# Optimization experiments

Hardware: AMD Instinct MI355X
Metric: run time of the kernel (lower is better)

The kernel has to match this reference:

```python
import jax, jax.numpy as jnp
import numpy as np

B, L, D = 1, 2048, 4096
H, KV, HD = 32, 8, 128
ROT = 64  # head_dim * partial_rotary_factor
SCALE = HD ** -0.5
NEG = -1e9


def _apply_rope(x, cos, sin):
    # x: [B, h, L, HD]; rotate only the first ROT dims (partial rotary, rotate-half convention)
    xr, xp = x[..., :ROT], x[..., ROT:]
    x1, x2 = jnp.split(xr, 2, axis=-1)
    rotated = jnp.concatenate([-x2, x1], axis=-1)
    xr = xr * cos[None, None] + rotated * sin[None, None]
    return jnp.concatenate([xr, xp], axis=-1)


def setup_inputs() -> dict:
    key = jax.random.key(0)
    k1, k2, k3 = jax.random.split(key, 3)
    x = jax.random.normal(k1, (B, L, D), jnp.float32)
    w_qkv = jax.random.normal(k2, (D, H * HD + 2 * KV * HD), jnp.float32) * 0.02
    w_o = jax.random.normal(k3, (H * HD, D), jnp.float32) * 0.02
    # causal additive mask, broadcast over batch and heads
    causal = jnp.tril(jnp.ones((L, L), dtype=bool))
    attention_mask = jnp.where(causal, 0.0, NEG).astype(jnp.float32)[None, None]
    # rotary tables over the ROT rotary dims
    inv_freq = 1.0 / (10000.0 ** (jnp.arange(0, ROT, 2, dtype=jnp.float32) / ROT))
    t = jnp.arange(L, dtype=jnp.float32)
    freqs = jnp.outer(t, inv_freq)            # [L, ROT/2]
    emb = jnp.concatenate([freqs, freqs], -1)  # [L, ROT]
    cos, sin = jnp.cos(emb), jnp.sin(emb)
    return {"x": x, "attention_mask": attention_mask, "cos": cos, "sin": sin,
            "w_qkv": w_qkv, "w_o": w_o}


def reference(x, attention_mask, cos, sin, w_qkv, w_o):
    Bx, Lx, _ = x.shape
    qkv = x @ w_qkv                                   # [B, L, H*HD + 2*KV*HD]
    q_pos = H * HD
    kv_pos = q_pos + KV * HD
    q = qkv[:, :, :q_pos].reshape(Bx, Lx, H, HD).transpose(0, 2, 1, 3)
    k = qkv[:, :, q_pos:kv_pos].reshape(Bx, Lx, KV, HD).transpose(0, 2, 1, 3)
    v = qkv[:, :, kv_pos:].reshape(Bx, Lx, KV, HD).transpose(0, 2, 1, 3)
    q = _apply_rope(q, cos, sin)
    k = _apply_rope(k, cos, sin)
    # GQA: duplicate KV heads (as in the original module)
    n_rep = H // KV
    k = jnp.repeat(k, n_rep, axis=1)
    v = jnp.repeat(v, n_rep, axis=1)
    w = jnp.einsum("bhqd,bhkd->bhqk", q, k) * SCALE   # [B, H, L, L]
    w = jax.nn.softmax(w + attention_mask, axis=-1)
    o = jnp.einsum("bhqk,bhkd->bhqd", w, v)           # [B, H, L, HD]
    o = o.transpose(0, 2, 1, 3).reshape(Bx, Lx, H * HD)
    return o @ w_o
```

## Files before the change

kernel.cpp:

```cpp
#include <hip/hip_runtime.h>
#include <stdint.h>

typedef float f32x4 __attribute__((ext_vector_type(4)));
typedef short s16x8 __attribute__((ext_vector_type(8)));
typedef unsigned short u16x4 __attribute__((ext_vector_type(4)));

#define SCALE_F 0.08838834764831845f

__device__ __forceinline__ unsigned short f32_to_bf16(float f) {
    union { float f; unsigned int u; } v; v.f = f;
    return (unsigned short)((v.u + 0x7FFFu + ((v.u >> 16) & 1u)) >> 16);
}

__device__ __forceinline__ void gload16(const void* g, void* l) {
    __builtin_amdgcn_global_load_lds((const __attribute__((address_space(1))) unsigned int*)g,
                                     (__attribute__((address_space(3))) unsigned int*)l,
                                     16, 0, 0);
}

__global__ void k_conv_bf16(const float* __restrict__ in, unsigned short* __restrict__ out, int n4) {
    int i = blockIdx.x * 256 + threadIdx.x;
    if (i >= n4) return;
    f32x4 v = ((const f32x4*)in)[i];
    u16x4 o;
    o[0] = f32_to_bf16(v[0]); o[1] = f32_to_bf16(v[1]);
    o[2] = f32_to_bf16(v[2]); o[3] = f32_to_bf16(v[3]);
    ((u16x4*)out)[i] = o;
}

__global__ void k_transpose_bf16(const float* __restrict__ in, unsigned short* __restrict__ out,
                                 int R, int in_ld, int in_off) {
    __shared__ float tile[64][65];
    const int rb = blockIdx.y * 64, cb = blockIdx.x * 64;
    const int t = threadIdx.x;
    const int lr = t >> 4, lc4 = (t & 15) * 4;
#pragma unroll
    for (int i = 0; i < 4; ++i) {
        int r = i * 16 + lr;
        f32x4 v = *(const f32x4*)(in + (size_t)(rb + r) * in_ld + in_off + cb + lc4);
        tile[r][lc4 + 0] = v[0]; tile[r][lc4 + 1] = v[1];
        tile[r][lc4 + 2] = v[2]; tile[r][lc4 + 3] = v[3];
    }
    __syncthreads();
#pragma unroll
    for (int i = 0; i < 4; ++i) {
        int oc = cb + i * 16 + lr;
        u16x4 o;
#pragma unroll
        for (int j = 0; j < 4; ++j)
            o[j] = f32_to_bf16(tile[lc4 + j][i * 16 + lr]);
        *(u16x4*)(out + (size_t)oc * R + rb + lc4) = o;
    }
}

template<int BN>
__global__ __launch_bounds__(512, 1)
void k_gemm8p(const unsigned short* __restrict__ A, const unsigned short* __restrict__ Bt,
              float* __restrict__ C, int N, int K) {
    constexpr int BH = BN * 32;
    constexpr int NF = BN / 64;
    __shared__ __align__(16) unsigned short As[2][2][8192];
    __shared__ __align__(16) unsigned short Bs[2][2][BH];
    const int tid = threadIdx.x;
    const int lane = tid & 63, wid = tid >> 6;
    const int g = lane >> 4, l15 = lane & 15;
    const int wm = wid >> 2, wn = wid & 3;
    const int nwg = gridDim.x, bid = blockIdx.x;
    const int swz = (bid & 7) * (nwg >> 3) + (bid >> 3);
    const int ntn = N / BN;
    const int bm = swz / ntn, bn = swz - bm * ntn;
    const int brow = bm << 8, bcol = bn * BN;

    const int rowS = ((tid >> 6) << 4) | (tid & 15);
    const int kcS = (tid >> 4) & 3;
    const unsigned short* sA = A + (size_t)(brow + rowS) * K + kcS * 8;
    const unsigned short* sB = Bt + (size_t)(bcol + rowS) * K + kcS * 8;

    f32x4 acc[8][NF] = {};
    const int nt = K >> 6;

    auto stA = [&](int t, int kh) {
        unsigned short* d = &As[t & 1][kh][tid * 8];
        const unsigned short* s = sA + (size_t)t * 64 + kh * 32;
        gload16(s, d);
        gload16(s + (size_t)128 * K, d + 4096);
    };
    auto stB = [&](int t, int kh) {
        unsigned short* d = &Bs[t & 1][kh][tid * 8];
        const unsigned short* s = sB + (size_t)t * 64 + kh * 32;
        gload16(s, d);
        if constexpr (BN == 256) gload16(s + (size_t)128 * K, d + 4096);
    };

    stA(0, 0); stB(0, 0); stA(0, 1); stB(0, 1);

    for (int t = 0; t < nt; ++t) {
        const int c = t & 1;
        if constexpr (BN == 256) {
            s16x8 af[4], bf[4];
            if (t + 1 < nt) { stA(t + 1, 0); asm volatile("s_waitcnt vmcnt(6)" ::: "memory"); }
            else            { asm volatile("s_waitcnt vmcnt(4)" ::: "memory"); }
            __builtin_amdgcn_s_barrier();
#pragma unroll
            for (int f = 0; f < 4; ++f)
                af[f] = *(const s16x8*)(&As[c][0][((wm * 8 + f) * 64 + g * 16 + l15) * 8]);
#pragma unroll
            for (int j = 0; j < 4; ++j)
                bf[j] = *(const s16x8*)(&Bs[c][0][((wn * 4 + j) * 64 + g * 16 + l15) * 8]);
            __builtin_amdgcn_s_setprio(1);
#pragma unroll
            for (int f = 0; f < 4; ++f)
#pragma unroll
                for (int j = 0; j < 4; ++j)
                    acc[f][j] = __builtin_amdgcn_mfma_f32_16x16x32_bf16(af[f], bf[j], acc[f][j], 0, 0, 0);
            __builtin_amdgcn_s_setprio(0);
            if (t + 1 < nt) stB(t + 1, 0);
#pragma unroll
            for (int f = 0; f < 4; ++f)
                af[f] = *(const s16x8*)(&As[c][0][((wm * 8 + 4 + f) * 64 + g * 16 + l15) * 8]);
            __builtin_amdgcn_s_setprio(1);
#pragma unroll
            for (int f = 0; f < 4; ++f)
#pragma unroll
                for (int j = 0; j < 4; ++j)
                    acc[4 + f][j] = __builtin_amdgcn_mfma_f32_16x16x32_bf16(af[f], bf[j], acc[4 + f][j], 0, 0, 0);
            __builtin_amdgcn_s_setprio(0);
            if (t + 1 < nt) { stA(t + 1, 1); asm volatile("s_waitcnt vmcnt(6)" ::: "memory"); }
            else            { asm volatile("s_waitcnt vmcnt(0)" ::: "memory"); }
            __builtin_amdgcn_s_barrier();
#pragma unroll
            for (int f = 0; f < 4; ++f)
                af[f] = *(const s16x8*)(&As[c][1][((wm * 8 + f) * 64 + g * 16 + l15) * 8]);
#pragma unroll
            for (int j = 0; j < 4; ++j)
                bf[j] = *(const s16x8*)(&Bs[c][1][((wn * 4 + j) * 64 + g * 16 + l15) * 8]);
            __builtin_amdgcn_s_setprio(1);
#pragma unroll
            for (int f = 0; f < 4; ++f)
#pragma unroll
                for (int j = 0; j < 4; ++j)
                    acc[f][j] = __builtin_amdgcn_mfma_f32_16x16x32_bf16(af[f], bf[j], acc[f][j], 0, 0, 0);
            __builtin_amdgcn_s_setprio(0);
            if (t + 1 < nt) stB(t + 1, 1);
#pragma unroll
            for (int f = 0; f < 4; ++f)
                af[f] = *(const s16x8*)(&As[c][1][((wm * 8 + 4 + f) * 64 + g * 16 + l15) * 8]);
            __builtin_amdgcn_s_setprio(1);
#pragma unroll
            for (int f = 0; f < 4; ++f)
#pragma unroll
                for (int j = 0; j < 4; ++j)
                    acc[4 + f][j] = __builtin_amdgcn_mfma_f32_16x16x32_bf16(af[f], bf[j], acc[4 + f][j], 0, 0, 0);
            __builtin_amdgcn_s_setprio(0);
        } else {
            s16x8 af[8], bf[2];
            if (t + 1 < nt) { stA(t + 1, 0); stB(t + 1, 0); asm volatile("s_waitcnt vmcnt(6)" ::: "memory"); }
            else            { asm volatile("s_waitcnt vmcnt(3)" ::: "memory"); }
            __builtin_amdgcn_s_barrier();
#pragma unroll
            for (int f = 0; f < 8; ++f)
                af[f] = *(const s16x8*)(&As[c][0][((wm * 8 + f) * 64 + g * 16 + l15) * 8]);
#pragma unroll
            for (int j = 0; j < 2; ++j)
                bf[j] = *(const s16x8*)(&Bs[c][0][((wn * 2 + j) * 64 + g * 16 + l15) * 8]);
            __builtin_amdgcn_s_setprio(1);
#pragma unroll
            for (int f = 0; f < 8; ++f)
#pragma unroll
                for (int j = 0; j < 2; ++j)
                    acc[f][j] = __builtin_amdgcn_mfma_f32_16x16x32_bf16(af[f], bf[j], acc[f][j], 0, 0, 0);
            __builtin_amdgcn_s_setprio(0);
            if (t + 1 < nt) { stA(t + 1, 1); stB(t + 1, 1); asm volatile("s_waitcnt vmcnt(6)" ::: "memory"); }
            else            { asm volatile("s_waitcnt vmcnt(0)" ::: "memory"); }
            __builtin_amdgcn_s_barrier();
#pragma unroll
            for (int f = 0; f < 8; ++f)
                af[f] = *(const s16x8*)(&As[c][1][((wm * 8 + f) * 64 + g * 16 + l15) * 8]);
#pragma unroll
            for (int j = 0; j < 2; ++j)
                bf[j] = *(const s16x8*)(&Bs[c][1][((wn * 2 + j) * 64 + g * 16 + l15) * 8]);
            __builtin_amdgcn_s_setprio(1);
#pragma unroll
            for (int f = 0; f < 8; ++f)
#pragma unroll
                for (int j = 0; j < 2; ++j)
                    acc[f][j] = __builtin_amdgcn_mfma_f32_16x16x32_bf16(af[f], bf[j], acc[f][j], 0, 0, 0);
            __builtin_amdgcn_s_setprio(0);
        }
    }

#pragma unroll
    for (int f = 0; f < 8; ++f)
#pragma unroll
        for (int j = 0; j < NF; ++j)
#pragma unroll
            for (int r = 0; r < 4; ++r)
                C[(size_t)(brow + wm * 128 + f * 16 + g * 4 + r) * N
                  + bcol + wn * (BN / 4) + j * 16 + l15] = acc[f][j][r];
}

__global__ void k_rope_pack(const float* __restrict__ qkv, const float* __restrict__ cosT,
                            const float* __restrict__ sinT, unsigned short* __restrict__ Qb,
                            unsigned short* __restrict__ Kb) {
    const int col = blockIdx.x * 256 + threadIdx.x;
    const int t = blockIdx.y;
    const float v = qkv[(size_t)t * 6144 + col];
    const int d = col & 127;
    float o = v;
    if (d < 64) {
        float c = cosT[t * 64 + d], s = sinT[t * 64 + d];
        float partner = qkv[(size_t)t * 6144 + ((d < 32) ? col + 32 : col - 32)];
        o = (d < 32) ? (v * c - partner * s) : (v * c + partner * s);
    }
    unsigned short ob = f32_to_bf16(o);
    if (col < 4096) {
        int h = col >> 7;
        Qb[((size_t)h * 2048 + t) * 128 + d] = ob;
    } else {
        int hk = (col - 4096) >> 7;
        Kb[((size_t)hk * 2048 + t) * 128 + d] = ob;
    }
}

__global__ __launch_bounds__(256, 2)
void k_attn(const unsigned short* __restrict__ Qb, const unsigned short* __restrict__ Kb,
            const unsigned short* __restrict__ Vt, unsigned short* __restrict__ Ob) {
    __shared__ __align__(16) unsigned short Ks[2][8192];
    __shared__ __align__(16) unsigned short Vs[2][8192];
    __shared__ __align__(16) unsigned short Pl[2][4][1024];
    const int h = blockIdx.y, hk = h >> 2;
    const int qbA = blockIdx.x, qbB = 31 - qbA;
    const int tid = threadIdx.x, lane = tid & 63, wid = tid >> 6;
    const int g = lane >> 4, l15 = lane & 15;
    const int qrA = qbA * 64 + wid * 16, qrB = qbB * 64 + wid * 16;
    const int swz = (l15 & 7) << 4;

    s16x8 aqA[4], aqB[4];
#pragma unroll
    for (int kc = 0; kc < 4; ++kc) {
        aqA[kc] = *(const s16x8*)(Qb + ((size_t)h * 2048 + qrA + l15) * 128 + kc * 32 + g * 8);
        aqB[kc] = *(const s16x8*)(Qb + ((size_t)h * 2048 + qrB + l15) * 128 + kc * 32 + g * 8);
    }

    const unsigned short* gK = Kb + ((size_t)hk * 2048 + (tid & 63)) * 128 + (tid >> 6) * 8;
    const unsigned short* gV = Vt + ((size_t)hk * 128 + (tid & 127)) * 2048 + (tid >> 7) * 8;

    auto stage = [&](int kb) {
        unsigned short* dK = Ks[kb & 1] + tid * 8;
        unsigned short* dV = Vs[kb & 1] + tid * 8;
        const unsigned short* sK = gK + (size_t)kb * 8192;
        const unsigned short* sV = gV + kb * 64;
#pragma unroll
        for (int i = 0; i < 4; ++i) gload16(sK + i * 32, dK + i * 2048);
#pragma unroll
        for (int i = 0; i < 4; ++i) gload16(sV + i * 16, dV + i * 2048);
    };

    f32x4 oaccA[8] = {}, oaccB[8] = {};
    float mA = -1e30f, lA = 0.f, mB = -1e30f, lB = 0.f;

    auto process = [&](const s16x8* aq, f32x4* oacc, float& mr, float& lr, int qrow0,
                       char* pw, const unsigned short* ks, const unsigned short* vs, int kb) {
        f32x4 s[4] = {};
#pragma unroll
        for (int kc = 0; kc < 4; ++kc)
#pragma unroll
            for (int kt = 0; kt < 4; ++kt) {
                s16x8 kf = *(const s16x8*)(ks + ((kc * 4 + g) * 64 + kt * 16 + l15) * 8);
                s[kt] = __builtin_amdgcn_mfma_f32_16x16x32_bf16(kf, aq[kc], s[kt], 0, 0, 0);
            }
        const int q = qrow0 + l15;
        if (kb * 64 + 63 > qrow0) {
#pragma unroll
            for (int kt = 0; kt < 4; ++kt)
#pragma unroll
                for (int r = 0; r < 4; ++r) {
                    float xv = s[kt][r] * SCALE_F;
                    s[kt][r] = (kb * 64 + kt * 16 + g * 4 + r > q) ? -3e38f : xv;
                }
        } else {
#pragma unroll
            for (int kt = 0; kt < 4; ++kt)
#pragma unroll
                for (int r = 0; r < 4; ++r) s[kt][r] *= SCALE_F;
        }
        float mx = -3e38f;
#pragma unroll
        for (int kt = 0; kt < 4; ++kt)
#pragma unroll
            for (int r = 0; r < 4; ++r) mx = fmaxf(mx, s[kt][r]);
        mx = fmaxf(mx, __shfl_xor(mx, 16));
        mx = fmaxf(mx, __shfl_xor(mx, 32));
        const float mnew = fmaxf(mr, mx);
        const float scal = __expf(mr - mnew);
        mr = mnew;
        float ps = 0.f;
#pragma unroll
        for (int kt = 0; kt < 4; ++kt)
#pragma unroll
            for (int r = 0; r < 4; ++r) {
                float p = __expf(s[kt][r] - mnew);
                s[kt][r] = p;
                ps += p;
            }
        ps += __shfl_xor(ps, 16);
        ps += __shfl_xor(ps, 32);
        lr = lr * scal + ps;
        float so[4];
#pragma unroll
        for (int r = 0; r < 4; ++r) so[r] = __shfl(scal, g * 4 + r, 16);
#pragma unroll
        for (int j = 0; j < 8; ++j) {
            oacc[j][0] *= so[0]; oacc[j][1] *= so[1];
            oacc[j][2] *= so[2]; oacc[j][3] *= so[3];
        }
#pragma unroll
        for (int kt = 0; kt < 4; ++kt) {
            unsigned int w0 = (unsigned int)f32_to_bf16(s[kt][0]) | ((unsigned int)f32_to_bf16(s[kt][1]) << 16);
            unsigned int w1 = (unsigned int)f32_to_bf16(s[kt][2]) | ((unsigned int)f32_to_bf16(s[kt][3]) << 16);
            const int b0 = (l15 * 128 + kt * 32 + g * 8) ^ swz;
            *(unsigned int*)(pw + b0) = w0;
            *(unsigned int*)(pw + b0 + 4) = w1;
        }
#pragma unroll
        for (int kc = 0; kc < 2; ++kc) {
            s16x8 pa = *(const s16x8*)(pw + ((l15 * 128 + kc * 64 + g * 16) ^ swz));
#pragma unroll
            for (int j = 0; j < 8; ++j) {
                s16x8 bv = *(const s16x8*)(vs + ((kc * 4 + g) * 128 + j * 16 + l15) * 8);
                oacc[j] = __builtin_amdgcn_mfma_f32_16x16x32_bf16(pa, bv, oacc[j], 0, 0, 0);
            }
        }
    };

    const int nkb = qbB + 1;
    stage(0);
    for (int kb = 0; kb < nkb; ++kb) {
        if (kb + 1 < nkb) {
            stage(kb + 1);
            asm volatile("s_waitcnt vmcnt(8)" ::: "memory");
        } else {
            asm volatile("s_waitcnt vmcnt(0)" ::: "memory");
        }
        __builtin_amdgcn_s_barrier();
        const unsigned short* ks = Ks[kb & 1];
        const unsigned short* vs = Vs[kb & 1];
        process(aqB, oaccB, mB, lB, qrB, (char*)Pl[1][wid], ks, vs, kb);
        if (kb <= qbA)
            process(aqA, oaccA, mA, lA, qrA, (char*)Pl[0][wid], ks, vs, kb);
        __builtin_amdgcn_s_barrier();
    }
    float liA[4], liB[4];
#pragma unroll
    for (int r = 0; r < 4; ++r) {
        liA[r] = 1.f / __shfl(lA, g * 4 + r, 16);
        liB[r] = 1.f / __shfl(lB, g * 4 + r, 16);
    }
#pragma unroll
    for (int j = 0; j < 8; ++j)
#pragma unroll
        for (int r = 0; r < 4; ++r) {
            Ob[(size_t)(qrA + g * 4 + r) * 4096 + h * 128 + j * 16 + l15] = f32_to_bf16(oaccA[j][r] * liA[r]);
            Ob[(size_t)(qrB + g * 4 + r) * 4096 + h * 128 + j * 16 + l15] = f32_to_bf16(oaccB[j][r] * liB[r]);
        }
}

extern "C" void kernel_launch(void* const* d_in, const int* in_sizes, int n_in,
                              void* d_out, int out_size, void* d_ws, size_t ws_size,
                              hipStream_t stream) {
    const float* x     = (const float*)d_in[0];
    const float* cosT  = (const float*)d_in[2];
    const float* sinT  = (const float*)d_in[3];
    const float* w_qkv = (const float*)d_in[4];
    const float* w_o   = (const float*)d_in[5];
    float* out = (float*)d_out;

    char* ws = (char*)d_ws;
    unsigned short* wT  = (unsigned short*)(ws + 0);
    float*          qkv = (float*)(ws + 50331648);
    unsigned short* Ob  = (unsigned short*)(ws + 50331648);
    unsigned short* xb  = (unsigned short*)(ws + 100663296);
    unsigned short* Qb  = xb;
    unsigned short* Kb  = (unsigned short*)(ws + 117440512);
    unsigned short* Vt  = (unsigned short*)(ws + 121634816);

    k_conv_bf16<<<8192, 256, 0, stream>>>(x, xb, 2097152);
    k_transpose_bf16<<<dim3(96, 64), 256, 0, stream>>>(w_qkv, wT, 4096, 6144, 0);
    k_gemm8p<256><<<192, 512, 0, stream>>>(xb, wT, qkv, 6144, 4096);
    k_rope_pack<<<dim3(20, 2048), 256, 0, stream>>>(qkv, cosT, sinT, Qb, Kb);
    k_transpose_bf16<<<dim3(16, 32), 256, 0, stream>>>(qkv, Vt, 2048, 6144, 5120);
    k_transpose_bf16<<<dim3(64, 64), 256, 0, stream>>>(w_o, wT, 4096, 4096, 0);
    k_attn<<<dim3(16, 32), 256, 0, stream>>>(Qb, Kb, Vt, Ob);
    k_gemm8p<128><<<256, 512, 0, stream>>>(Ob, wT, out, 4096, 4096);
}
```

Measured before the change: 428.0 us.

## Restructure GEMM pipelines with barrier-fenced MFMA phases and 128x256 output tiles

```diff
diff --git a/kernel.cpp b/kernel.cpp
--- a/kernel.cpp
+++ b/kernel.cpp
@@ -53,30 +53,27 @@
     }
 }
 
-template<int BN>
 __global__ __launch_bounds__(512, 1)
-void k_gemm8p(const unsigned short* __restrict__ A, const unsigned short* __restrict__ Bt,
-              float* __restrict__ C, int N, int K) {
-    constexpr int BH = BN * 32;
-    constexpr int NF = BN / 64;
+void k_gemmA(const unsigned short* __restrict__ A, const unsigned short* __restrict__ Bt,
+             float* __restrict__ C, int N, int K) {
     __shared__ __align__(16) unsigned short As[2][2][8192];
-    __shared__ __align__(16) unsigned short Bs[2][2][BH];
+    __shared__ __align__(16) unsigned short Bs[2][2][8192];
     const int tid = threadIdx.x;
     const int lane = tid & 63, wid = tid >> 6;
     const int g = lane >> 4, l15 = lane & 15;
     const int wm = wid >> 2, wn = wid & 3;
     const int nwg = gridDim.x, bid = blockIdx.x;
     const int swz = (bid & 7) * (nwg >> 3) + (bid >> 3);
-    const int ntn = N / BN;
+    const int ntn = N >> 8;
     const int bm = swz / ntn, bn = swz - bm * ntn;
-    const int brow = bm << 8, bcol = bn * BN;
+    const int brow = bm << 8, bcol = bn << 8;
 
     const int rowS = ((tid >> 6) << 4) | (tid & 15);
     const int kcS = (tid >> 4) & 3;
     const unsigned short* sA = A + (size_t)(brow + rowS) * K + kcS * 8;
     const unsigned short* sB = Bt + (size_t)(bcol + rowS) * K + kcS * 8;
 
-    f32x4 acc[8][NF] = {};
+    f32x4 acc[8][4] = {};
     const int nt = K >> 6;
 
     auto stA = [&](int t, int kh) {
@@ -89,24 +86,143 @@
         unsigned short* d = &Bs[t & 1][kh][tid * 8];
         const unsigned short* s = sB + (size_t)t * 64 + kh * 32;
         gload16(s, d);
-        if constexpr (BN == 256) gload16(s + (size_t)128 * K, d + 4096);
+        gload16(s + (size_t)128 * K, d + 4096);
     };
 
     stA(0, 0); stB(0, 0); stA(0, 1); stB(0, 1);
+    asm volatile("s_waitcnt vmcnt(4)" ::: "memory");
+    __builtin_amdgcn_s_barrier();
 
     for (int t = 0; t < nt; ++t) {
         const int c = t & 1;
-        if constexpr (BN == 256) {
+        s16x8 af[4], bf[4];
+#pragma unroll
+        for (int f = 0; f < 4; ++f)
+            af[f] = *(const s16x8*)(&As[c][0][((wm * 8 + f) * 64 + g * 16 + l15) * 8]);
+#pragma unroll
+        for (int j = 0; j < 4; ++j)
+            bf[j] = *(const s16x8*)(&Bs[c][0][((wn * 4 + j) * 64 + g * 16 + l15) * 8]);
+        if (t + 1 < nt) stA(t + 1, 0);
+        __builtin_amdgcn_s_barrier();
+        __builtin_amdgcn_sched_barrier(0);
+        __builtin_amdgcn_s_setprio(1);
+#pragma unroll
+        for (int f = 0; f < 4; ++f)
+#pragma unroll
+            for (int j = 0; j < 4; ++j)
+                acc[f][j] = __builtin_amdgcn_mfma_f32_16x16x32_bf16(af[f], bf[j], acc[f][j], 0, 0, 0);
+        __builtin_amdgcn_s_setprio(0);
+        __builtin_amdgcn_s_barrier();
+#pragma unroll
+        for (int f = 0; f < 4; ++f)
+            af[f] = *(const s16x8*)(&As[c][0][((wm * 8 + 4 + f) * 64 + g * 16 + l15) * 8]);
+        if (t + 1 < nt) { stB(t + 1, 0); asm volatile("s_waitcnt vmcnt(4)" ::: "memory"); }
+        else            { asm volatile("s_waitcnt vmcnt(0)" ::: "memory"); }
+        __builtin_amdgcn_s_barrier();
+        __builtin_amdgcn_sched_barrier(0);
+        __builtin_amdgcn_s_setprio(1);
+#pragma unroll
+        for (int f = 0; f < 4; ++f)
+#pragma unroll
+            for (int j = 0; j < 4; ++j)
+                acc[4 + f][j] = __builtin_amdgcn_mfma_f32_16x16x32_bf16(af[f], bf[j], acc[4 + f][j], 0, 0, 0);
+        __builtin_amdgcn_s_setprio(0);
+        __builtin_amdgcn_s_barrier();
+#pragma unroll
+        for (int f = 0; f < 4; ++f)
+            af[f] = *(const s16x8*)(&As[c][1][((wm * 8 + f) * 64 + g * 16 + l15) * 8]);
+#pragma unroll
+        for (int j = 0; j < 4; ++j)
+            bf[j] = *(const s16x8*)(&Bs[c][1][((wn * 4 + j) * 64 + g * 16 + l15) * 8]);
+        if (t + 1 < nt) stA(t + 1, 1);
+        __builtin_amdgcn_s_barrier();
+        __builtin_amdgcn_sched_barrier(0);
+        __builtin_amdgcn_s_setprio(1);
+#pragma unroll
+        for (int f = 0; f < 4; ++f)
+#pragma unroll
+            for (int j = 0; j < 4; ++j)
+                acc[f][j] = __builtin_amdgcn_mfma_f32_16x16x32_bf16(af[f], bf[j], acc[f][j], 0, 0, 0);
+        __builtin_amdgcn_s_setprio(0);
+        __builtin_amdgcn_s_barrier();
+#pragma unroll
+        for (int f = 0; f < 4; ++f)
+            af[f] = *(const s16x8*)(&As[c][1][((wm * 8 + 4 + f) * 64 + g * 16 + l15) * 8]);
+        if (t + 1 < nt) { stB(t + 1, 1); asm volatile("s_waitcnt vmcnt(4)" ::: "memory"); }
+        __builtin_amdgcn_s_barrier();
+        __builtin_amdgcn_sched_barrier(0);
+        __builtin_amdgcn_s_setprio(1);
+#pragma unroll
+        for (int f = 0; f < 4; ++f)
+#pragma unroll
+            for (int j = 0; j < 4; ++j)
+                acc[4 + f][j] = __builtin_amdgcn_mfma_f32_16x16x32_bf16(af[f], bf[j], acc[4 + f][j], 0, 0, 0);
+        __builtin_amdgcn_s_setprio(0);
+        __builtin_amdgcn_s_barrier();
+    }
+
+#pragma unroll
+    for (int f = 0; f < 8; ++f)
+#pragma unroll
+        for (int j = 0; j < 4; ++j)
+#pragma unroll
+            for (int r = 0; r < 4; ++r)
+                C[(size_t)(brow + wm * 128 + f * 16 + g * 4 + r) * N
+                  + bcol + wn * 64 + j * 16 + l15] = acc[f][j][r];
+}
+
+__global__ __launch_bounds__(512, 1)
+void k_gemmB(const unsigned short* __restrict__ A, const unsigned short* __restrict__ Bt,
+             float* __restrict__ C, int N, int K) {
+    __shared__ __align__(16) unsigned short As[2][2][4096];
+    __shared__ __align__(16) unsigned short Bs[2][2][8192];
+    const int tid = threadIdx.x;
+    const int lane = tid & 63, wid = tid >> 6;
+    const int g = lane >> 4, l15 = lane & 15;
+    const int wm = wid >> 2, wn = wid & 3;
+    const int nwg = gridDim.x, bid = blockIdx.x;
+    const int swz = (bid & 7) * (nwg >> 3) + (bid >> 3);
+    const int ntn = N >> 8;
+    const int bm = swz / ntn, bn = swz - bm * ntn;
+    const int brow = bm << 7, bcol = bn << 8;
+
+    const int rowS = ((tid >> 6) << 4) | (tid & 15);
+    const int kcS = (tid >> 4) & 3;
+    const unsigned short* sA = A + (size_t)(brow + rowS) * K + kcS * 8;
+    const unsigned short* sB = Bt + (size_t)(bcol + rowS) * K + kcS * 8;
+
+    f32x4 acc[4][4] = {};
+    const int nt = K >> 6;
+
+    auto stg = [&](int t, int kh) {
+        unsigned short* dA = &As[t & 1][kh][tid * 8];
+        unsigned short* dB = &Bs[t & 1][kh][tid * 8];
+        const unsigned short* srcA = sA + (size_t)t * 64 + kh * 32;
+        const unsigned short* srcB = sB + (size_t)t * 64 + kh * 32;
+        gload16(srcA, dA);
+        gload16(srcB, dB);
+        gload16(srcB + (size_t)128 * K, dB + 4096);
+    };
+
+    stg(0, 0); stg(0, 1);
+    asm volatile("s_waitcnt vmcnt(3)" ::: "memory");
+    __builtin_amdgcn_s_barrier();
+
+    for (int t = 0; t < nt; ++t) {
+        const int c = t & 1;
+#pragma unroll
+        for (int kh = 0; kh < 2; ++kh) {
             s16x8 af[4], bf[4];
-            if (t + 1 < nt) { stA(t + 1, 0); asm volatile("s_waitcnt vmcnt(6)" ::: "memory"); }
-            else            { asm volatile("s_waitcnt vmcnt(4)" ::: "memory"); }
+#pragma unroll
+            for (int f = 0; f < 4; ++f)
+                af[f] = *(const s16x8*)(&As[c][kh][((wm * 4 + f) * 64 + g * 16 + l15) * 8]);
+#pragma unroll
+            for (int j = 0; j < 4; ++j)
+                bf[j] = *(const s16x8*)(&Bs[c][kh][((wn * 4 + j) * 64 + g * 16 + l15) * 8]);
+            if (t + 1 < nt) { stg(t + 1, kh); asm volatile("s_waitcnt vmcnt(3)" ::: "memory"); }
+            else if (kh == 0) { asm volatile("s_waitcnt vmcnt(0)" ::: "memory"); }
             __builtin_amdgcn_s_barrier();
-#pragma unroll
-            for (int f = 0; f < 4; ++f)
-                af[f] = *(const s16x8*)(&As[c][0][((wm * 8 + f) * 64 + g * 16 + l15) * 8]);
-#pragma unroll
-            for (int j = 0; j < 4; ++j)
-                bf[j] = *(const s16x8*)(&Bs[c][0][((wn * 4 + j) * 64 + g * 16 + l15) * 8]);
+            __builtin_amdgcn_sched_barrier(0);
             __builtin_amdgcn_s_setprio(1);
 #pragma unroll
             for (int f = 0; f < 4; ++f)
@@ -114,89 +230,18 @@
                 for (int j = 0; j < 4; ++j)
                     acc[f][j] = __builtin_amdgcn_mfma_f32_16x16x32_bf16(af[f], bf[j], acc[f][j], 0, 0, 0);
             __builtin_amdgcn_s_setprio(0);
-            if (t + 1 < nt) stB(t + 1, 0);
-#pragma unroll
-            for (int f = 0; f < 4; ++f)
-                af[f] = *(const s16x8*)(&As[c][0][((wm * 8 + 4 + f) * 64 + g * 16 + l15) * 8]);
-            __builtin_amdgcn_s_setprio(1);
-#pragma unroll
-            for (int f = 0; f < 4; ++f)
-#pragma unroll
-                for (int j = 0; j < 4; ++j)
-                    acc[4 + f][j] = __builtin_amdgcn_mfma_f32_16x16x32_bf16(af[f], bf[j], acc[4 + f][j], 0, 0, 0);
-            __builtin_amdgcn_s_setprio(0);
-            if (t + 1 < nt) { stA(t + 1, 1); asm volatile("s_waitcnt vmcnt(6)" ::: "memory"); }
-            else            { asm volatile("s_waitcnt vmcnt(0)" ::: "memory"); }
             __builtin_amdgcn_s_barrier();
-#pragma unroll
-            for (int f = 0; f < 4; ++f)
-                af[f] = *(const s16x8*)(&As[c][1][((wm * 8 + f) * 64 + g * 16 + l15) * 8]);
-#pragma unroll
-            for (int j = 0; j < 4; ++j)
-                bf[j] = *(const s16x8*)(&Bs[c][1][((wn * 4 + j) * 64 + g * 16 + l15) * 8]);
-            __builtin_amdgcn_s_setprio(1);
-#pragma unroll
-            for (int f = 0; f < 4; ++f)
-#pragma unroll
-                for (int j = 0; j < 4; ++j)
-                    acc[f][j] = __builtin_amdgcn_mfma_f32_16x16x32_bf16(af[f], bf[j], acc[f][j], 0, 0, 0);
-            __builtin_amdgcn_s_setprio(0);
-            if (t + 1 < nt) stB(t + 1, 1);
-#pragma unroll
-            for (int f = 0; f < 4; ++f)
-                af[f] = *(const s16x8*)(&As[c][1][((wm * 8 + 4 + f) * 64 + g * 16 + l15) * 8]);
-            __builtin_amdgcn_s_setprio(1);
-#pragma unroll
-            for (int f = 0; f < 4; ++f)
-#pragma unroll
-                for (int j = 0; j < 4; ++j)
-                    acc[4 + f][j] = __builtin_amdgcn_mfma_f32_16x16x32_bf16(af[f], bf[j], acc[4 + f][j], 0, 0, 0);
-            __builtin_amdgcn_s_setprio(0);
-        } else {
-            s16x8 af[8], bf[2];
-            if (t + 1 < nt) { stA(t + 1, 0); stB(t + 1, 0); asm volatile("s_waitcnt vmcnt(6)" ::: "memory"); }
-            else            { asm volatile("s_waitcnt vmcnt(3)" ::: "memory"); }
-            __builtin_amdgcn_s_barrier();
-#pragma unroll
-            for (int f = 0; f < 8; ++f)
-                af[f] = *(const s16x8*)(&As[c][0][((wm * 8 + f) * 64 + g * 16 + l15) * 8]);
-#pragma unroll
-            for (int j = 0; j < 2; ++j)
-                bf[j] = *(const s16x8*)(&Bs[c][0][((wn * 2 + j) * 64 + g * 16 + l15) * 8]);
-            __builtin_amdgcn_s_setprio(1);
-#pragma unroll
-            for (int f = 0; f < 8; ++f)
-#pragma unroll
-                for (int j = 0; j < 2; ++j)
-                    acc[f][j] = __builtin_amdgcn_mfma_f32_16x16x32_bf16(af[f], bf[j], acc[f][j], 0, 0, 0);
-            __builtin_amdgcn_s_setprio(0);
-            if (t + 1 < nt) { stA(t + 1, 1); stB(t + 1, 1); asm volatile("s_waitcnt vmcnt(6)" ::: "memory"); }
-            else            { asm volatile("s_waitcnt vmcnt(0)" ::: "memory"); }
-            __builtin_amdgcn_s_barrier();
-#pragma unroll
-            for (int f = 0; f < 8; ++f)
-                af[f] = *(const s16x8*)(&As[c][1][((wm * 8 + f) * 64 + g * 16 + l15) * 8]);
-#pragma unroll
-            for (int j = 0; j < 2; ++j)
-                bf[j] = *(const s16x8*)(&Bs[c][1][((wn * 2 + j) * 64 + g * 16 + l15) * 8]);
-            __builtin_amdgcn_s_setprio(1);
-#pragma unroll
-            for (int f = 0; f < 8; ++f)
-#pragma unroll
-                for (int j = 0; j < 2; ++j)
-                    acc[f][j] = __builtin_amdgcn_mfma_f32_16x16x32_bf16(af[f], bf[j], acc[f][j], 0, 0, 0);
-            __builtin_amdgcn_s_setprio(0);
-        }
-    }
-
-#pragma unroll
-    for (int f = 0; f < 8; ++f)
-#pragma unroll
-        for (int j = 0; j < NF; ++j)
+        }
+    }
+
+#pragma unroll
+    for (int f = 0; f < 4; ++f)
+#pragma unroll
+        for (int j = 0; j < 4; ++j)
 #pragma unroll
             for (int r = 0; r < 4; ++r)
-                C[(size_t)(brow + wm * 128 + f * 16 + g * 4 + r) * N
-                  + bcol + wn * (BN / 4) + j * 16 + l15] = acc[f][j][r];
+                C[(size_t)(brow + wm * 64 + f * 16 + g * 4 + r) * N
+                  + bcol + wn * 64 + j * 16 + l15] = acc[f][j][r];
 }
 
 __global__ void k_rope_pack(const float* __restrict__ qkv, const float* __restrict__ cosT,
@@ -386,10 +431,10 @@
 
     k_conv_bf16<<<8192, 256, 0, stream>>>(x, xb, 2097152);
     k_transpose_bf16<<<dim3(96, 64), 256, 0, stream>>>(w_qkv, wT, 4096, 6144, 0);
-    k_gemm8p<256><<<192, 512, 0, stream>>>(xb, wT, qkv, 6144, 4096);
+    k_gemmA<<<192, 512, 0, stream>>>(xb, wT, qkv, 6144, 4096);
     k_rope_pack<<<dim3(20, 2048), 256, 0, stream>>>(qkv, cosT, sinT, Qb, Kb);
     k_transpose_bf16<<<dim3(16, 32), 256, 0, stream>>>(qkv, Vt, 2048, 6144, 5120);
     k_transpose_bf16<<<dim3(64, 64), 256, 0, stream>>>(w_o, wT, 4096, 4096, 0);
     k_attn<<<dim3(16, 32), 256, 0, stream>>>(Qb, Kb, Vt, Ob);
-    k_gemm8p<128><<<256, 512, 0, stream>>>(Ob, wT, out, 4096, 4096);
-}
+    k_gemmB<<<256, 512, 0, stream>>>(Ob, wT, out, 4096, 4096);
+}
```

New measurement: 435.2 us. Within noise of the previous version (+1.7%).
